# Optimization experiments

Hardware: AMD Instinct MI355X
Metric: run time of the kernel (lower is better)

Reference implementation:

```python
import jax, jax.numpy as jnp
import numpy as np

D_MODEL = 1024
NHEAD = 16
HEAD_DIM = D_MODEL // NHEAD


def setup_inputs() -> dict:
    key = jax.random.key(0)
    ks = jax.random.split(key, 7)
    B, S = 4, 2048
    scale = 1.0 / np.sqrt(D_MODEL)
    x = jax.random.normal(ks[0], (B, S, D_MODEL), dtype=jnp.float32)
    Wq = jax.random.normal(ks[1], (D_MODEL, D_MODEL), dtype=jnp.float32) * scale
    Wk = jax.random.normal(ks[2], (D_MODEL, D_MODEL), dtype=jnp.float32) * scale
    Wv = jax.random.normal(ks[3], (D_MODEL, D_MODEL), dtype=jnp.float32) * scale
    bq = jax.random.normal(ks[4], (D_MODEL,), dtype=jnp.float32) * 0.01
    bk = jax.random.normal(ks[5], (D_MODEL,), dtype=jnp.float32) * 0.01
    bv = jax.random.normal(ks[6], (D_MODEL,), dtype=jnp.float32) * 0.01
    return {"x": x, "Wq": Wq, "bq": bq, "Wk": Wk, "bk": bk, "Wv": Wv, "bv": bv}


def reference(x, Wq, bq, Wk, bk, Wv, bv):
    B, S, _ = x.shape
    # Linear projections (torch Linear: x @ W.T + b; weights here are already [in, out])
    q = x @ Wq + bq
    k = x @ Wk + bk
    v = x @ Wv + bv
    # [B, S, H, Dh] -> [B, H, S, Dh]
    q = q.reshape(B, S, NHEAD, HEAD_DIM).transpose(0, 2, 1, 3)
    k = k.reshape(B, S, NHEAD, HEAD_DIM).transpose(0, 2, 1, 3)
    v = v.reshape(B, S, NHEAD, HEAD_DIM).transpose(0, 2, 1, 3)
    # NOTE: original scales by sqrt(d_model), not sqrt(head_dim)
    scores = jnp.einsum("bhqd,bhkd->bhqk", q, k) / np.sqrt(D_MODEL).astype(np.float32)
    attn = jax.nn.softmax(scores, axis=-1)  # dropout is identity at eval
    out = jnp.einsum("bhqk,bhkd->bhqd", attn, v)
    out = out.transpose(0, 2, 1, 3).reshape(B, S, D_MODEL)
    return out
```

## Files before the change

### kernel.cpp

```cpp
#include <hip/hip_runtime.h>
#include <cstdint>
#include <cstddef>

#define SEQ 2048
#define BATCH 4
#define KVB 64
#define NT (SEQ / KVB)

typedef __attribute__((ext_vector_type(8))) unsigned short u16x8;
typedef __attribute__((ext_vector_type(8))) __bf16 bf16x8;
typedef __attribute__((ext_vector_type(4))) float f32x4;
typedef __attribute__((ext_vector_type(4))) unsigned short u16x4;

#if defined(__has_builtin)
#if __has_builtin(__builtin_amdgcn_exp2f)
#define EXP2(x) __builtin_amdgcn_exp2f(x)
#else
#define EXP2(x) exp2f(x)
#endif
#else
#define EXP2(x) exp2f(x)
#endif

static __device__ __forceinline__ unsigned short f2bf(float f) {
  unsigned u = __builtin_bit_cast(unsigned, f);
  u += 0x7fffu + ((u >> 16) & 1u);
  return (unsigned short)(u >> 16);
}

static __device__ __forceinline__ f32x4 mfma16(u16x8 a, u16x8 b, f32x4 c) {
  return __builtin_amdgcn_mfma_f32_16x16x32_bf16(
      __builtin_bit_cast(bf16x8, a), __builtin_bit_cast(bf16x8, b), c, 0, 0, 0);
}

static __device__ __forceinline__ f32x4 mfma16b(u16x8 a, bf16x8 b, f32x4 c) {
  return __builtin_amdgcn_mfma_f32_16x16x32_bf16(
      __builtin_bit_cast(bf16x8, a), b, c, 0, 0, 0);
}

static __device__ __forceinline__ void gl_lds16(const void* g, void* l) {
  __builtin_amdgcn_global_load_lds(
      (const __attribute__((address_space(1))) void*)g,
      (__attribute__((address_space(3))) void*)l, 16, 0, 0);
}

__global__ __launch_bounds__(256) void k_conv_x(const float* __restrict__ x,
                                                unsigned short* __restrict__ xb) {
  int i = (blockIdx.x * 256 + threadIdx.x) * 8;
  f32x4 a = *reinterpret_cast<const f32x4*>(x + i);
  f32x4 b = *reinterpret_cast<const f32x4*>(x + i + 4);
  u16x8 v;
  v[0] = f2bf(a[0]); v[1] = f2bf(a[1]); v[2] = f2bf(a[2]); v[3] = f2bf(a[3]);
  v[4] = f2bf(b[0]); v[5] = f2bf(b[1]); v[6] = f2bf(b[2]); v[7] = f2bf(b[3]);
  *reinterpret_cast<u16x8*>(xb + i) = v;
}

__global__ __launch_bounds__(256) void k_conv_w(const float* __restrict__ Wq,
                                                const float* __restrict__ Wk,
                                                const float* __restrict__ Wv,
                                                unsigned short* __restrict__ wt) {
  const float* W = (blockIdx.z == 0) ? Wq : (blockIdx.z == 1) ? Wk : Wv;
  unsigned short* dst = wt + (size_t)blockIdx.z * 1024 * 1024;
  __shared__ float tile[32][33];
  int n0 = blockIdx.x * 32, k0 = blockIdx.y * 32;
  int tx = threadIdx.x, ty = threadIdx.y;
#pragma unroll
  for (int i = 0; i < 4; i++) {
    int k = ty + i * 8;
    tile[k][tx] = W[(size_t)(k0 + k) * 1024 + n0 + tx];
  }
  __syncthreads();
#pragma unroll
  for (int i = 0; i < 4; i++) {
    int n = ty + i * 8;
    dst[(size_t)(n0 + n) * 1024 + k0 + tx] = f2bf(tile[tx][n]);
  }
}

__global__ __launch_bounds__(256) void k_qkv_gemm(
    const unsigned short* __restrict__ xb, const unsigned short* __restrict__ wt,
    const float* __restrict__ bq, const float* __restrict__ bk,
    const float* __restrict__ bv,
    unsigned short* __restrict__ qb, unsigned short* __restrict__ kb,
    unsigned short* __restrict__ vt) {
  __shared__ unsigned short Ah[3][128 * 32];
  __shared__ unsigned short Bh[3][128 * 32];
  const int tid = threadIdx.x;
  const int lane = tid & 63, wid = tid >> 6;
  const int ln = lane & 15, g = lane >> 4;
  const int wr = wid >> 1, wc = wid & 1;
  const int dd = blockIdx.x;
  const int xcd = dd & 7, j = dd >> 3;
  const int z = j >> 6, kk = j & 63;
  const int m0 = (((kk >> 3) << 3) | xcd) * 128;
  const int n0 = (kk & 7) * 128;
  const unsigned short* Bt = wt + (size_t)z * 1024 * 1024;

  f32x4 acc[4][4];
#pragma unroll
  for (int i = 0; i < 4; i++)
#pragma unroll
    for (int jj = 0; jj < 4; jj++) acc[i][jj] = f32x4{0.f, 0.f, 0.f, 0.f};

  const int rA0 = tid >> 2, cA0 = tid & 3;
  const int swA = (cA0 ^ ((rA0 >> 1) & 3)) << 3;
  const int rA1 = rA0 + 64;

  const unsigned short* gA0 = xb + (size_t)(m0 + rA0) * 1024 + swA;
  const unsigned short* gA1 = xb + (size_t)(m0 + rA1) * 1024 + swA;
  const unsigned short* gB0 = Bt + (size_t)(n0 + rA0) * 1024 + swA;
  const unsigned short* gB1 = Bt + (size_t)(n0 + rA1) * 1024 + swA;

#define GSTAGE(bb, k0)                                          \
  do {                                                          \
    gl_lds16(gA0 + (k0), &Ah[bb][wid * 512]);                   \
    gl_lds16(gA1 + (k0), &Ah[bb][2048 + wid * 512]);            \
    gl_lds16(gB0 + (k0), &Bh[bb][wid * 512]);                   \
    gl_lds16(gB1 + (k0), &Bh[bb][2048 + wid * 512]);            \
  } while (0)

  const int fsw = (g ^ ((ln >> 1) & 3)) << 3;

#define GCOMPUTE(bb)                                                       \
  do {                                                                     \
    u16x8 af[4], bfv[4];                                                   \
    _Pragma("unroll") for (int mi = 0; mi < 4; mi++)                       \
      af[mi] = *reinterpret_cast<const u16x8*>(                            \
          &Ah[bb][(wr * 64 + mi * 16 + ln) * 32 + fsw]);                   \
    _Pragma("unroll") for (int ni = 0; ni < 4; ni++)                       \
      bfv[ni] = *reinterpret_cast<const u16x8*>(                           \
          &Bh[bb][(wc * 64 + ni * 16 + ln) * 32 + fsw]);                   \
    __builtin_amdgcn_s_setprio(1);                                         \
    _Pragma("unroll") for (int mi = 0; mi < 4; mi++)                       \
    _Pragma("unroll") for (int ni = 0; ni < 4; ni++)                       \
      acc[mi][ni] = mfma16(af[mi], bfv[ni], acc[mi][ni]);                  \
    __builtin_amdgcn_s_setprio(0);                                         \
  } while (0)

  GSTAGE(0, 0);
  GSTAGE(1, 32);
  asm volatile("s_waitcnt vmcnt(4)" ::: "memory");
  __builtin_amdgcn_s_barrier();

  for (int t = 0; t < 30; t++) {
    GSTAGE((t + 2) % 3, (t + 2) * 32);
    GCOMPUTE(t % 3);
    asm volatile("s_waitcnt vmcnt(4)" ::: "memory");
    __builtin_amdgcn_s_barrier();
  }
  GCOMPUTE(0);
  asm volatile("s_waitcnt vmcnt(0)" ::: "memory");
  __builtin_amdgcn_s_barrier();
  GCOMPUTE(1);

  const float* bias = (z == 0) ? bq : (z == 1) ? bk : bv;
#pragma unroll
  for (int ni = 0; ni < 4; ni++) {
    int n = n0 + wc * 64 + ni * 16 + ln;
    float bb = bias[n];
    int h = n >> 6, d = n & 63;
#pragma unroll
    for (int mi = 0; mi < 4; mi++) {
      int mb = m0 + wr * 64 + mi * 16 + 4 * g;
      int b = mb >> 11, s = mb & 2047;
      if (z == 2) {
        u16x4 pv;
#pragma unroll
        for (int i = 0; i < 4; i++) pv[i] = f2bf(acc[mi][ni][i] + bb);
        int s4 = s >> 2;
        int u = s4 & 7, blk = s4 >> 3;
        int nu = ((u & 3) << 1) | (u >> 2);
        int sp = ((blk << 3) | nu) << 2;
        *reinterpret_cast<u16x4*>(
            &vt[((size_t)((b * 16 + h) * 64 + d)) * 2048 + sp]) = pv;
      } else {
        unsigned short* dst = (z == 0) ? qb : kb;
        float sc = (z == 0) ? 0.0450842200f : 1.0f;
#pragma unroll
        for (int i = 0; i < 4; i++) {
          dst[((size_t)((b * 16 + h) * 2048) + (s + i)) * 64 + d] =
              f2bf((acc[mi][ni][i] + bb) * sc);
        }
      }
    }
  }
#undef GSTAGE
#undef GCOMPUTE
}

__global__ __launch_bounds__(512) void k_attn(
    const unsigned short* __restrict__ qb, const unsigned short* __restrict__ kb,
    const unsigned short* __restrict__ vt, float* __restrict__ out) {
  __shared__ unsigned short Kl[3][KVB * 64];
  __shared__ unsigned short Vl[3][64 * KVB];
  const int tid = threadIdx.x;
  const int lane = tid & 63, wid = tid >> 6;
  const int ln = lane & 15, g = lane >> 4;
  const int flat = blockIdx.x;
  const int bh = flat & 63, qidx = flat >> 6;
  const int b = bh >> 4, h = bh & 15;
  const int q0 = qidx * 256 + wid * 32;
  const unsigned short* Qp = qb + (size_t)bh * SEQ * 64;
  const unsigned short* Kp = kb + (size_t)bh * SEQ * 64;
  const unsigned short* Vp = vt + (size_t)bh * 64 * SEQ;

  const int kr0 = tid >> 3;
  const int psw = ((tid & 7) ^ (kr0 & 7)) << 3;
  const unsigned short* srcK0 = Kp + (size_t)kr0 * 64 + psw;
  const unsigned short* srcV0 = Vp + (size_t)kr0 * SEQ + psw;

#define STAGE(bb, tt)                                                     \
  do {                                                                    \
    gl_lds16(srcK0 + (size_t)(tt) * (KVB * 64), &Kl[bb][wid * 512]);      \
    gl_lds16(srcV0 + (size_t)(tt) * KVB, &Vl[bb][wid * 512]);             \
  } while (0)

  u16x8 qf[2][2];
#pragma unroll
  for (int qt = 0; qt < 2; qt++)
#pragma unroll
    for (int dc = 0; dc < 2; dc++)
      qf[qt][dc] = *reinterpret_cast<const u16x8*>(
          &Qp[(size_t)(q0 + qt * 16 + ln) * 64 + dc * 32 + g * 8]);

  f32x4 o[4][2];
#pragma unroll
  for (int dt = 0; dt < 4; dt++)
#pragma unroll
    for (int qt = 0; qt < 2; qt++) o[dt][qt] = f32x4{0.f, 0.f, 0.f, 0.f};
  f32x4 lsum[2] = {f32x4{0.f, 0.f, 0.f, 0.f}, f32x4{0.f, 0.f, 0.f, 0.f}};

  u16x8 ones;
#pragma unroll
  for (int i = 0; i < 8; i++) ones[i] = 0x3F80;

  const int lm = ln & 7;
  const int ksw0 = (g ^ lm) << 3;
  const int ksw1 = ((4 + g) ^ lm) << 3;
  const int vsw0 = (g ^ lm) << 3;
  const int vsw1 = ((4 + g) ^ lm) << 3;

#define ACOMPUTE(bi)                                                          \
  do {                                                                        \
    const unsigned short* Kb = Kl[bi];                                        \
    const unsigned short* Vb = Vl[bi];                                        \
    u16x8 kf[4][2];                                                           \
    _Pragma("unroll") for (int kt = 0; kt < 4; kt++) {                        \
      int rb = (kt * 16 + ln) * 64;                                           \
      kf[kt][0] = *reinterpret_cast<const u16x8*>(&Kb[rb + ksw0]);            \
      kf[kt][1] = *reinterpret_cast<const u16x8*>(&Kb[rb + ksw1]);            \
    }                                                                         \
    f32x4 st[2][4];                                                           \
    __builtin_amdgcn_s_setprio(1);                                            \
    _Pragma("unroll") for (int qt = 0; qt < 2; qt++)                          \
    _Pragma("unroll") for (int kt = 0; kt < 4; kt++) {                        \
      f32x4 c = f32x4{0.f, 0.f, 0.f, 0.f};                                    \
      c = mfma16(kf[kt][0], qf[qt][0], c);                                    \
      c = mfma16(kf[kt][1], qf[qt][1], c);                                    \
      st[qt][kt] = c;                                                         \
    }                                                                         \
    __builtin_amdgcn_s_setprio(0);                                            \
    _Pragma("unroll") for (int qt = 0; qt < 2; qt++)                          \
    _Pragma("unroll") for (int kt = 0; kt < 4; kt++)                          \
    _Pragma("unroll") for (int i = 0; i < 4; i++)                             \
      st[qt][kt][i] = EXP2(st[qt][kt][i]);                                    \
    bf16x8 pb[2][2];                                                          \
    _Pragma("unroll") for (int qt = 0; qt < 2; qt++)                          \
    _Pragma("unroll") for (int ks = 0; ks < 2; ks++)                          \
    _Pragma("unroll") for (int i = 0; i < 4; i++) {                           \
      pb[qt][ks][i] = (__bf16)st[qt][2 * ks][i];                              \
      pb[qt][ks][4 + i] = (__bf16)st[qt][2 * ks + 1][i];                      \
    }                                                                         \
    __builtin_amdgcn_s_setprio(1);                                            \
    _Pragma("unroll") for (int dt = 0; dt < 4; dt++) {                        \
      int rb = (dt * 16 + ln) * 64;                                           \
      u16x8 vf0 = *reinterpret_cast<const u16x8*>(&Vb[rb + vsw0]);            \
      o[dt][0] = mfma16b(vf0, pb[0][0], o[dt][0]);                            \
      o[dt][1] = mfma16b(vf0, pb[1][0], o[dt][1]);                            \
      u16x8 vf1 = *reinterpret_cast<const u16x8*>(&Vb[rb + vsw1]);            \
      o[dt][0] = mfma16b(vf1, pb[0][1], o[dt][0]);                            \
      o[dt][1] = mfma16b(vf1, pb[1][1], o[dt][1]);                            \
    }                                                                         \
    _Pragma("unroll") for (int ks = 0; ks < 2; ks++) {                        \
      lsum[0] = mfma16b(ones, pb[0][ks], lsum[0]);                            \
      lsum[1] = mfma16b(ones, pb[1][ks], lsum[1]);                            \
    }                                                                         \
    __builtin_amdgcn_s_setprio(0);                                            \
  } while (0)

  STAGE(0, 0);
  STAGE(1, 1);
  asm volatile("s_waitcnt vmcnt(2)" ::: "memory");
  __builtin_amdgcn_s_barrier();

  for (int t = 0; t < NT - 2; t++) {
    STAGE((t + 2) % 3, t + 2);
    ACOMPUTE(t % 3);
    asm volatile("s_waitcnt vmcnt(2)" ::: "memory");
    __builtin_amdgcn_s_barrier();
  }
  ACOMPUTE((NT - 2) % 3);
  asm volatile("s_waitcnt vmcnt(0)" ::: "memory");
  __builtin_amdgcn_s_barrier();
  ACOMPUTE((NT - 1) % 3);

  float inv[2] = {1.f / lsum[0][0], 1.f / lsum[1][0]};

#pragma unroll
  for (int qt = 0; qt < 2; qt++) {
    int q = q0 + qt * 16 + ln;
#pragma unroll
    for (int dt = 0; dt < 4; dt++) {
      f32x4 r;
#pragma unroll
      for (int i = 0; i < 4; i++) r[i] = o[dt][qt][i] * inv[qt];
      *reinterpret_cast<f32x4*>(
          &out[((size_t)(b * SEQ + q)) * 1024 + h * 64 + dt * 16 + 4 * g]) = r;
    }
  }
#undef STAGE
#undef ACOMPUTE
}

extern "C" void kernel_launch(void* const* d_in, const int* in_sizes, int n_in,
                              void* d_out, int out_size, void* d_ws, size_t ws_size,
                              hipStream_t stream) {
  (void)in_sizes; (void)n_in; (void)out_size;
  const float* x  = (const float*)d_in[0];
  const float* Wq = (const float*)d_in[1];
  const float* bq = (const float*)d_in[2];
  const float* Wk = (const float*)d_in[3];
  const float* bk = (const float*)d_in[4];
  const float* Wv = (const float*)d_in[5];
  const float* bv = (const float*)d_in[6];
  float* out = (float*)d_out;

  char* ws = (char*)d_ws;
  if (ws_size < 73400320u) return;
  unsigned short* xb    = (unsigned short*)(ws);
  unsigned short* wt    = (unsigned short*)(ws + 16777216);
  unsigned short* qbuf  = (unsigned short*)(ws + 23068672);
  unsigned short* kbuf  = (unsigned short*)(ws + 39845888);
  unsigned short* vtbuf = (unsigned short*)(ws + 56623104);

  k_conv_x<<<4096, 256, 0, stream>>>(x, xb);
  k_conv_w<<<dim3(32, 32, 3), dim3(32, 8), 0, stream>>>(Wq, Wk, Wv, wt);
  k_qkv_gemm<<<dim3(1536), 256, 0, stream>>>(xb, wt, bq, bk, bv,
                                             qbuf, kbuf, vtbuf);
  k_attn<<<dim3(512), dim3(512), 0, stream>>>(qbuf, kbuf, vtbuf, out);
}
```

Measured before the change: 165.9 us.

## Double per-wave query rows in attention and reorder GEMM stage/compute

Each attention wave now handles 64 query rows instead of 32, so each K/V tile loaded into LDS is reused across twice as many queries and the grid halves to 256 blocks. The QK^T/exp step runs in two halves to bound register pressure. Separately, the QKV GEMM loop now issues its compute before the next global-to-LDS stage load. This trades fewer K/V loads and barriers for more registers per wave and only 256 blocks, which may leave some of the MI355X's compute units idle.

Measured after the change: 156.8 us. 5.5% less time.

```diff
diff --git a/kernel.cpp b/kernel.cpp
--- a/kernel.cpp
+++ b/kernel.cpp
@@ -143,8 +143,8 @@
   __builtin_amdgcn_s_barrier();
 
   for (int t = 0; t < 30; t++) {
+    GCOMPUTE(t % 3);
     GSTAGE((t + 2) % 3, (t + 2) * 32);
-    GCOMPUTE(t % 3);
     asm volatile("s_waitcnt vmcnt(4)" ::: "memory");
     __builtin_amdgcn_s_barrier();
   }
@@ -199,7 +199,7 @@
   const int flat = blockIdx.x;
   const int bh = flat & 63, qidx = flat >> 6;
   const int b = bh >> 4, h = bh & 15;
-  const int q0 = qidx * 256 + wid * 32;
+  const int q0 = qidx * 512 + wid * 64;
   const unsigned short* Qp = qb + (size_t)bh * SEQ * 64;
   const unsigned short* Kp = kb + (size_t)bh * SEQ * 64;
   const unsigned short* Vp = vt + (size_t)bh * 64 * SEQ;
@@ -215,20 +215,22 @@
     gl_lds16(srcV0 + (size_t)(tt) * KVB, &Vl[bb][wid * 512]);             \
   } while (0)
 
-  u16x8 qf[2][2];
-#pragma unroll
-  for (int qt = 0; qt < 2; qt++)
+  u16x8 qf[4][2];
+#pragma unroll
+  for (int qt = 0; qt < 4; qt++)
 #pragma unroll
     for (int dc = 0; dc < 2; dc++)
       qf[qt][dc] = *reinterpret_cast<const u16x8*>(
           &Qp[(size_t)(q0 + qt * 16 + ln) * 64 + dc * 32 + g * 8]);
 
-  f32x4 o[4][2];
+  f32x4 o[4][4];
 #pragma unroll
   for (int dt = 0; dt < 4; dt++)
 #pragma unroll
-    for (int qt = 0; qt < 2; qt++) o[dt][qt] = f32x4{0.f, 0.f, 0.f, 0.f};
-  f32x4 lsum[2] = {f32x4{0.f, 0.f, 0.f, 0.f}, f32x4{0.f, 0.f, 0.f, 0.f}};
+    for (int qt = 0; qt < 4; qt++) o[dt][qt] = f32x4{0.f, 0.f, 0.f, 0.f};
+  f32x4 lsum[4];
+#pragma unroll
+  for (int qt = 0; qt < 4; qt++) lsum[qt] = f32x4{0.f, 0.f, 0.f, 0.f};
 
   u16x8 ones;
 #pragma unroll
@@ -250,41 +252,42 @@
       kf[kt][0] = *reinterpret_cast<const u16x8*>(&Kb[rb + ksw0]);            \
       kf[kt][1] = *reinterpret_cast<const u16x8*>(&Kb[rb + ksw1]);            \
     }                                                                         \
-    f32x4 st[2][4];                                                           \
-    __builtin_amdgcn_s_setprio(1);                                            \
-    _Pragma("unroll") for (int qt = 0; qt < 2; qt++)                          \
-    _Pragma("unroll") for (int kt = 0; kt < 4; kt++) {                        \
-      f32x4 c = f32x4{0.f, 0.f, 0.f, 0.f};                                    \
-      c = mfma16(kf[kt][0], qf[qt][0], c);                                    \
-      c = mfma16(kf[kt][1], qf[qt][1], c);                                    \
-      st[qt][kt] = c;                                                         \
-    }                                                                         \
-    __builtin_amdgcn_s_setprio(0);                                            \
-    _Pragma("unroll") for (int qt = 0; qt < 2; qt++)                          \
-    _Pragma("unroll") for (int kt = 0; kt < 4; kt++)                          \
-    _Pragma("unroll") for (int i = 0; i < 4; i++)                             \
-      st[qt][kt][i] = EXP2(st[qt][kt][i]);                                    \
-    bf16x8 pb[2][2];                                                          \
-    _Pragma("unroll") for (int qt = 0; qt < 2; qt++)                          \
-    _Pragma("unroll") for (int ks = 0; ks < 2; ks++)                          \
-    _Pragma("unroll") for (int i = 0; i < 4; i++) {                           \
-      pb[qt][ks][i] = (__bf16)st[qt][2 * ks][i];                              \
-      pb[qt][ks][4 + i] = (__bf16)st[qt][2 * ks + 1][i];                      \
+    bf16x8 pb[4][2];                                                          \
+    _Pragma("unroll") for (int half = 0; half < 2; half++) {                  \
+      f32x4 st[2][4];                                                         \
+      __builtin_amdgcn_s_setprio(1);                                          \
+      _Pragma("unroll") for (int q2 = 0; q2 < 2; q2++)                        \
+      _Pragma("unroll") for (int kt = 0; kt < 4; kt++) {                      \
+        f32x4 c = f32x4{0.f, 0.f, 0.f, 0.f};                                  \
+        c = mfma16(kf[kt][0], qf[half * 2 + q2][0], c);                       \
+        c = mfma16(kf[kt][1], qf[half * 2 + q2][1], c);                       \
+        st[q2][kt] = c;                                                       \
+      }                                                                       \
+      __builtin_amdgcn_s_setprio(0);                                          \
+      _Pragma("unroll") for (int q2 = 0; q2 < 2; q2++)                        \
+      _Pragma("unroll") for (int kt = 0; kt < 4; kt++)                        \
+      _Pragma("unroll") for (int i = 0; i < 4; i++)                           \
+        st[q2][kt][i] = EXP2(st[q2][kt][i]);                                  \
+      _Pragma("unroll") for (int q2 = 0; q2 < 2; q2++)                        \
+      _Pragma("unroll") for (int ks = 0; ks < 2; ks++)                        \
+      _Pragma("unroll") for (int i = 0; i < 4; i++) {                         \
+        pb[half * 2 + q2][ks][i] = (__bf16)st[q2][2 * ks][i];                 \
+        pb[half * 2 + q2][ks][4 + i] = (__bf16)st[q2][2 * ks + 1][i];         \
+      }                                                                       \
     }                                                                         \
     __builtin_amdgcn_s_setprio(1);                                            \
     _Pragma("unroll") for (int dt = 0; dt < 4; dt++) {                        \
       int rb = (dt * 16 + ln) * 64;                                           \
       u16x8 vf0 = *reinterpret_cast<const u16x8*>(&Vb[rb + vsw0]);            \
-      o[dt][0] = mfma16b(vf0, pb[0][0], o[dt][0]);                            \
-      o[dt][1] = mfma16b(vf0, pb[1][0], o[dt][1]);                            \
+      _Pragma("unroll") for (int qt = 0; qt < 4; qt++)                        \
+        o[dt][qt] = mfma16b(vf0, pb[qt][0], o[dt][qt]);                       \
       u16x8 vf1 = *reinterpret_cast<const u16x8*>(&Vb[rb + vsw1]);            \
-      o[dt][0] = mfma16b(vf1, pb[0][1], o[dt][0]);                            \
-      o[dt][1] = mfma16b(vf1, pb[1][1], o[dt][1]);                            \
+      _Pragma("unroll") for (int qt = 0; qt < 4; qt++)                        \
+        o[dt][qt] = mfma16b(vf1, pb[qt][1], o[dt][qt]);                       \
     }                                                                         \
-    _Pragma("unroll") for (int ks = 0; ks < 2; ks++) {                        \
-      lsum[0] = mfma16b(ones, pb[0][ks], lsum[0]);                            \
-      lsum[1] = mfma16b(ones, pb[1][ks], lsum[1]);                            \
-    }                                                                         \
+    _Pragma("unroll") for (int ks = 0; ks < 2; ks++)                          \
+    _Pragma("unroll") for (int qt = 0; qt < 4; qt++)                          \
+      lsum[qt] = mfma16b(ones, pb[qt][ks], lsum[qt]);                         \
     __builtin_amdgcn_s_setprio(0);                                            \
   } while (0)
 
@@ -304,16 +307,15 @@
   __builtin_amdgcn_s_barrier();
   ACOMPUTE((NT - 1) % 3);
 
-  float inv[2] = {1.f / lsum[0][0], 1.f / lsum[1][0]};
-
-#pragma unroll
-  for (int qt = 0; qt < 2; qt++) {
+#pragma unroll
+  for (int qt = 0; qt < 4; qt++) {
+    float inv = 1.f / lsum[qt][0];
     int q = q0 + qt * 16 + ln;
 #pragma unroll
     for (int dt = 0; dt < 4; dt++) {
       f32x4 r;
 #pragma unroll
-      for (int i = 0; i < 4; i++) r[i] = o[dt][qt][i] * inv[qt];
+      for (int i = 0; i < 4; i++) r[i] = o[dt][qt][i] * inv;
       *reinterpret_cast<f32x4*>(
           &out[((size_t)(b * SEQ + q)) * 1024 + h * 64 + dt * 16 + 4 * g]) = r;
     }
@@ -347,5 +349,5 @@
   k_conv_w<<<dim3(32, 32, 3), dim3(32, 8), 0, stream>>>(Wq, Wk, Wv, wt);
   k_qkv_gemm<<<dim3(1536), 256, 0, stream>>>(xb, wt, bq, bk, bv,
                                              qbuf, kbuf, vtbuf);
-  k_attn<<<dim3(512), dim3(512), 0, stream>>>(qbuf, kbuf, vtbuf, out);
-}
+  k_attn<<<dim3(256), dim3(512), 0, stream>>>(qbuf, kbuf, vtbuf, out);
+}
```
